# Kernel tuning notes

Hardware: AMD Instinct MI355X
Metric: run time of the kernel (lower is better)

## Reference

```python
import jax, jax.numpy as jnp
import numpy as np

B, H, W, D = 2, 64, 64, 512
D_HEAD = 64
N_HEADS = D // D_HEAD
KERNEL = 7


def make_neighbourhood_mask(kernel: int, canvas_h: int, canvas_w: int) -> jnp.ndarray:
    """Boolean [HW, HW] mask: query (i,j) attends to a clamped kernel x kernel window."""
    h_ramp = jnp.arange(canvas_h)
    w_ramp = jnp.arange(canvas_w)
    h_pos, w_pos = jnp.meshgrid(h_ramp, w_ramp, indexing='ij')
    start_h = jnp.clip(h_pos - kernel // 2, 0, canvas_h - kernel)[..., None, None]
    end_h = start_h + kernel
    start_w = jnp.clip(w_pos - kernel // 2, 0, canvas_w - kernel)[..., None, None]
    end_w = start_w + kernel
    h_range = h_ramp.reshape(1, 1, canvas_h, 1)
    w_range = w_ramp.reshape(1, 1, 1, canvas_w)
    mask = (h_range >= start_h) & (h_range < end_h) & (w_range >= start_w) & (w_range < end_w)
    return mask.reshape(canvas_h * canvas_w, canvas_h * canvas_w)


def setup_inputs() -> dict:
    key = jax.random.key(0)
    k1, k2, k3 = jax.random.split(key, 3)
    x = jax.random.normal(k1, (B, H, W, D), dtype=jnp.float32)
    w_qkv = jax.random.normal(k2, (3 * D, D), dtype=jnp.float32) * (D ** -0.5)
    w_out = jax.random.normal(k3, (D, D), dtype=jnp.float32) * (D ** -0.5)
    return {"x": x, "w_qkv": w_qkv, "w_out": w_out}


def reference(x, w_qkv, w_out):
    b, h, w, d = x.shape
    s = h * w
    # qkv projection (Linear, no bias): [b,h,w,3d]
    qkv = jnp.einsum('bhwd,ed->bhwe', x, w_qkv)
    # split per torch rearrange 'n h w (t nh e) -> t n nh (h w) e'
    qkv = qkv.reshape(b, s, 3, N_HEADS, D_HEAD).transpose(2, 0, 3, 1, 4)  # [3,b,nh,s,e]
    q, k, v = qkv[0], qkv[1], qkv[2]
    mask = make_neighbourhood_mask(KERNEL, h, w)  # [s, s] bool
    scale = D_HEAD ** -0.5
    scores = jnp.einsum('bnse,bnte->bnst', q, k) * scale  # [b,nh,s,s]
    neg_inf = jnp.finfo(scores.dtype).min
    scores = jnp.where(mask[None, None, :, :], scores, neg_inf)
    attn = jax.nn.softmax(scores, axis=-1)
    out = jnp.einsum('bnst,bnte->bnse', attn, v)  # [b,nh,s,e]
    out = out.transpose(0, 2, 1, 3).reshape(b, h, w, d)  # [b,h,w,d]
    return jnp.einsum('bhwd,ed->bhwe', out, w_out)
```

## Files before the change

kernel.cpp:

```cpp
#include <hip/hip_runtime.h>
#include <hip/hip_bf16.h>


typedef __bf16 bf16x8 __attribute__((ext_vector_type(8)));
typedef __bf16 bf16x4 __attribute__((ext_vector_type(4)));
typedef float  f32x4  __attribute__((ext_vector_type(4)));

__global__ __launch_bounds__(256) void cvt_w(
    const float* __restrict__ wq, const float* __restrict__ wo,
    __bf16* __restrict__ wqb, __bf16* __restrict__ wob) {
  int i = blockIdx.x * 256 + threadIdx.x;
  const float* src;
  __bf16* dst;
  int j = i;
  if (j < 196608) {
    src = wq; dst = wqb;
  } else {
    j -= 196608; src = wo; dst = wob;
  }
  f32x4 v = ((const f32x4*)src)[j];
  bf16x4 o;
  o[0] = (__bf16)v[0]; o[1] = (__bf16)v[1];
  o[2] = (__bf16)v[2]; o[3] = (__bf16)v[3];
  ((bf16x4*)dst)[j] = o;
}

__device__ __forceinline__ void gload_lds16(const __bf16* g, __bf16* l) {
  __builtin_amdgcn_global_load_lds(
      (const __attribute__((address_space(1))) void*)g,
      (__attribute__((address_space(3))) void*)l, 16, 0, 0);
}

__global__ __launch_bounds__(256, 3) void gemm_qkv(
    const float* __restrict__ A, const __bf16* __restrict__ W,
    __bf16* __restrict__ qo, __bf16* __restrict__ ko, __bf16* __restrict__ vo,
    int etiles) {
  constexpr int K = 512;
  __shared__ alignas(16) __bf16 Al[128][36];
  __shared__ alignas(16) __bf16 Wl[128 * 32];
  const int tid = threadIdx.x;
  const int wv = tid >> 6, lane = tid & 63;
  const int n16 = lane & 15, quad = lane >> 4;
  const int bi = blockIdx.x / etiles, be = blockIdx.x % etiles;
  const int i0 = bi << 7, e0 = be << 7;
  const int wm = (wv & 1) << 6, we = (wv >> 1) << 6;

  const int arow = tid >> 1, ahalf = tid & 1;
  const float* gA = A + (size_t)(i0 + arow) * K + ahalf * 16;
  const int srow = (wv << 4) + (lane >> 2);
  const int scol = (lane & 3) << 3;
  const __bf16* gW = W + (size_t)(e0 + srow) * K + scol;
  __bf16* lW = &Wl[(wv << 9) + (lane << 3)];

  f32x4 acc[4][4];
#pragma unroll
  for (int a = 0; a < 4; ++a)
#pragma unroll
    for (int b = 0; b < 4; ++b) acc[a][b] = (f32x4){0.f, 0.f, 0.f, 0.f};

  f32x4 a4[4];
#pragma unroll
  for (int j = 0; j < 4; ++j) a4[j] = *(const f32x4*)(gA + j * 4);

  for (int k0 = 0; k0 < K; k0 += 32) {
    bf16x8 ab0, ab1;
#pragma unroll
    for (int j = 0; j < 4; ++j) {
      ab0[j] = (__bf16)a4[0][j]; ab0[j + 4] = (__bf16)a4[1][j];
      ab1[j] = (__bf16)a4[2][j]; ab1[j + 4] = (__bf16)a4[3][j];
    }
    if (k0) __syncthreads();
    *(bf16x8*)&Al[arow][ahalf * 16] = ab0;
    *(bf16x8*)&Al[arow][ahalf * 16 + 8] = ab1;
    gload_lds16(gW + k0, lW);
    gload_lds16(gW + (size_t)64 * K + k0, lW + 64 * 32);
    if (k0 + 32 < K) {
#pragma unroll
      for (int j = 0; j < 4; ++j)
        a4[j] = *(const f32x4*)(gA + k0 + 32 + j * 4);
    }
    __syncthreads();

    bf16x8 af[4], wf[4];
#pragma unroll
    for (int t = 0; t < 4; ++t) {
      af[t] = *(const bf16x8*)&Al[wm + t * 16 + n16][quad * 8];
      wf[t] = *(const bf16x8*)&Wl[(we + t * 16 + n16) * 32 + quad * 8];
    }
#pragma unroll
    for (int mt = 0; mt < 4; ++mt)
#pragma unroll
      for (int nt = 0; nt < 4; ++nt)
        acc[mt][nt] = __builtin_amdgcn_mfma_f32_16x16x32_bf16(
            af[mt], wf[nt], acc[mt][nt], 0, 0, 0);
  }

#pragma unroll
  for (int mt = 0; mt < 4; ++mt)
#pragma unroll
    for (int nt = 0; nt < 4; ++nt) {
      f32x4 f = acc[mt][nt];
      int e = e0 + we + nt * 16 + n16;
      int t = e >> 9, head = (e >> 6) & 7, dh = e & 63;
      int ib = i0 + wm + mt * 16 + quad * 4;
      int b = ib >> 12, s = ib & 4095;
      int bh = b * 8 + head;
      if (t == 2) {
        __bf16* p = vo + ((size_t)bh * 64 + dh) * 4096 + s;
#pragma unroll
        for (int rg = 0; rg < 4; ++rg) p[rg] = (__bf16)f[rg];
      } else {
        __bf16* p = ((t == 0) ? qo : ko) + ((size_t)bh * 4096 + s) * 64 + dh;
#pragma unroll
        for (int rg = 0; rg < 4; ++rg) p[rg * 64] = (__bf16)f[rg];
      }
    }
}

__global__ __launch_bounds__(256, 3) void gemm_out(
    const __bf16* __restrict__ A, const __bf16* __restrict__ W,
    float* __restrict__ co, int etiles) {
  constexpr int K = 512;
  __shared__ alignas(16) __bf16 Al[128 * 32];
  __shared__ alignas(16) __bf16 Wl[64 * 32];
  const int tid = threadIdx.x;
  const int wv = tid >> 6, lane = tid & 63;
  const int n16 = lane & 15, quad = lane >> 4;
  const int bi = blockIdx.x / etiles, be = blockIdx.x % etiles;
  const int i0 = bi << 7, e0 = be << 6;
  const int wm = (wv & 1) << 6, we = (wv >> 1) << 5;

  const int srow = (wv << 4) + (lane >> 2);
  const int scol = (lane & 3) << 3;
  const __bf16* gA = A + (size_t)(i0 + srow) * K + scol;
  const __bf16* gW = W + (size_t)(e0 + srow) * K + scol;
  __bf16* lA = &Al[(wv << 9) + (lane << 3)];
  __bf16* lW = &Wl[(wv << 9) + (lane << 3)];

  f32x4 acc[4][2];
#pragma unroll
  for (int a = 0; a < 4; ++a)
#pragma unroll
    for (int b = 0; b < 2; ++b) acc[a][b] = (f32x4){0.f, 0.f, 0.f, 0.f};

  for (int k0 = 0; k0 < K; k0 += 32) {
    if (k0) __syncthreads();
    gload_lds16(gA + k0, lA);
    gload_lds16(gA + (size_t)64 * K + k0, lA + 64 * 32);
    gload_lds16(gW + k0, lW);
    __syncthreads();

    bf16x8 af[4], wf[2];
#pragma unroll
    for (int t = 0; t < 4; ++t)
      af[t] = *(const bf16x8*)&Al[(wm + t * 16 + n16) * 32 + quad * 8];
#pragma unroll
    for (int t = 0; t < 2; ++t)
      wf[t] = *(const bf16x8*)&Wl[(we + t * 16 + n16) * 32 + quad * 8];
#pragma unroll
    for (int mt = 0; mt < 4; ++mt)
#pragma unroll
      for (int nt = 0; nt < 2; ++nt)
        acc[mt][nt] = __builtin_amdgcn_mfma_f32_16x16x32_bf16(
            af[mt], wf[nt], acc[mt][nt], 0, 0, 0);
  }

#pragma unroll
  for (int mt = 0; mt < 4; ++mt)
#pragma unroll
    for (int nt = 0; nt < 2; ++nt) {
      f32x4 f = acc[mt][nt];
      int e = e0 + we + nt * 16 + n16;
      int ib = i0 + wm + mt * 16 + quad * 4;
      float* p = co + (size_t)ib * 512 + e;
#pragma unroll
      for (int rg = 0; rg < 4; ++rg) p[rg * 512] = f[rg];
    }
}

__global__ __launch_bounds__(256) void attn_mfma(
    const __bf16* __restrict__ q, const __bf16* __restrict__ k,
    const __bf16* __restrict__ vt, __bf16* __restrict__ out) {
  __shared__ alignas(16) __bf16 r1[14848];
  __shared__ alignas(16) __bf16 sbuf[4][16][232];
  const int tid = threadIdx.x;
  const int wv = tid >> 6;
  const int lane = tid & 63;
  const int n16 = lane & 15, quad = lane >> 4;
  const int bh = blockIdx.x >> 6;
  const int tile = blockIdx.x & 63;
  const int qh0 = (tile >> 3) << 3, qw0 = (tile & 7) << 3;
  int wh0 = qh0 - 3; wh0 = wh0 < 0 ? 0 : (wh0 > 50 ? 50 : wh0);
  int wc0 = qw0 - 3; wc0 = wc0 < 0 ? 0 : (wc0 > 48 ? 48 : wc0);
  wc0 &= ~1;
  const size_t base = (size_t)bh * 4096 * 64;

  const int qi_a = wv * 16 + n16;
  const int sqa = (qh0 + (qi_a >> 3)) * 64 + qw0 + (qi_a & 7);
  const __bf16* qp = q + base + (size_t)sqa * 64 + quad * 8;
  bf16x8 aq0 = *(const bf16x8*)qp;
  bf16x8 aq1 = *(const bf16x8*)(qp + 32);

  const __bf16* kbase = k + base;
#pragma unroll
  for (int i = 0; i < 7; ++i) {
    int ch = i * 256 + tid;
    int kr = ch >> 7, wi = ch & 127;
    int kc = wi >> 3, dh8 = wi & 7;
    bf16x8 d = *(const bf16x8*)(kbase +
        (size_t)((wh0 + kr) * 64 + wc0 + kc) * 64 + dh8 * 8);
    *(bf16x8*)&r1[(kr * 16 + kc) * 64 + ((dh8 ^ (kc & 7)) * 8)] = d;
  }
  __syncthreads();

  f32x4 S[14];
  const int skw = wc0 + n16;
  const int sw1 = ((quad ^ (n16 & 7)) * 8);
  const int sw2 = (((4 + quad) ^ (n16 & 7)) * 8);
#pragma unroll
  for (int nt = 0; nt < 14; ++nt) {
    int key = nt * 16 + n16;
    bf16x8 b0 = *(const bf16x8*)&r1[key * 64 + sw1];
    bf16x8 b1 = *(const bf16x8*)&r1[key * 64 + sw2];
    f32x4 s = {0.f, 0.f, 0.f, 0.f};
    s = __builtin_amdgcn_mfma_f32_16x16x32_bf16(aq0, b0, s, 0, 0, 0);
    s = __builtin_amdgcn_mfma_f32_16x16x32_bf16(aq1, b1, s, 0, 0, 0);
    S[nt] = s;
  }

  float mx[4] = {-1e30f, -1e30f, -1e30f, -1e30f};
#pragma unroll
  for (int reg = 0; reg < 4; ++reg) {
    int qi = wv * 16 + quad * 4 + reg;
    int qh = qh0 + (qi >> 3), qw = qw0 + (qi & 7);
    int sh = qh - 3; sh = sh < 0 ? 0 : (sh > 57 ? 57 : sh);
    int sw = qw - 3; sw = sw < 0 ? 0 : (sw > 57 ? 57 : sw);
    bool wok = (skw >= sw) && (skw < sw + 7);
#pragma unroll
    for (int nt = 0; nt < 14; ++nt) {
      int kh = wh0 + nt;
      bool ok = wok && (kh >= sh) && (kh < sh + 7);
      float val = ok ? S[nt][reg] * 0.125f : -1e30f;
      S[nt][reg] = val;
      mx[reg] = mx[reg] > val ? mx[reg] : val;
    }
  }
#pragma unroll
  for (int reg = 0; reg < 4; ++reg)
#pragma unroll
    for (int off = 8; off >= 1; off >>= 1) {
      float o = __shfl_xor(mx[reg], off);
      mx[reg] = mx[reg] > o ? mx[reg] : o;
    }

  float sm[4] = {0.f, 0.f, 0.f, 0.f};
#pragma unroll
  for (int nt = 0; nt < 14; ++nt)
#pragma unroll
    for (int reg = 0; reg < 4; ++reg) {
      float p = __expf(S[nt][reg] - mx[reg]);
      S[nt][reg] = p;
      sm[reg] += p;
    }
#pragma unroll
  for (int reg = 0; reg < 4; ++reg)
#pragma unroll
    for (int off = 8; off >= 1; off >>= 1) sm[reg] += __shfl_xor(sm[reg], off);

#pragma unroll
  for (int reg = 0; reg < 4; ++reg) {
    float inv = 1.f / sm[reg];
    int row = quad * 4 + reg;
#pragma unroll
    for (int nt = 0; nt < 14; ++nt)
      sbuf[wv][row][nt * 16 + n16] = (__bf16)(S[nt][reg] * inv);
  }

  __syncthreads();
  const __bf16* vtb = vt + base;
#pragma unroll
  for (int i = 0; i < 7; ++i) {
    int c = i * 256 + tid;
    int dh = c / 28, rem = c % 28;
    int kr = rem >> 1, half = rem & 1;
    bf16x8 d = *(const bf16x8*)(vtb + (size_t)dh * 4096 +
                                (wh0 + kr) * 64 + wc0 + half * 8);
    *(bf16x8*)&r1[dh * 232 + kr * 16 + half * 8] = d;
  }
  __syncthreads();

  f32x4 O[4] = {{0.f, 0.f, 0.f, 0.f},
                {0.f, 0.f, 0.f, 0.f},
                {0.f, 0.f, 0.f, 0.f},
                {0.f, 0.f, 0.f, 0.f}};
#pragma unroll
  for (int kt = 0; kt < 7; ++kt) {
    bf16x8 pa = *(const bf16x8*)&sbuf[wv][n16][kt * 32 + quad * 8];
    int key0 = kt * 32 + quad * 8;
#pragma unroll
    for (int ntv = 0; ntv < 4; ++ntv) {
      bf16x8 vb = *(const bf16x8*)&r1[(ntv * 16 + n16) * 232 + key0];
      O[ntv] = __builtin_amdgcn_mfma_f32_16x16x32_bf16(pa, vb, O[ntv], 0, 0, 0);
    }
  }

  const int b = bh >> 3, head = bh & 7;
#pragma unroll
  for (int ntv = 0; ntv < 4; ++ntv)
#pragma unroll
    for (int reg = 0; reg < 4; ++reg) {
      int qi = wv * 16 + quad * 4 + reg;
      int s_q = (qh0 + (qi >> 3)) * 64 + qw0 + (qi & 7);
      int dh = ntv * 16 + n16;
      out[((size_t)(b * 4096 + s_q)) * 512 + head * 64 + dh] =
          (__bf16)O[ntv][reg];
    }
}

extern "C" void kernel_launch(void* const* d_in, const int* in_sizes, int n_in,
                              void* d_out, int out_size, void* d_ws,
                              size_t ws_size, hipStream_t stream) {
  const float* x = (const float*)d_in[0];
  const float* w_qkv = (const float*)d_in[1];
  const float* w_out = (const float*)d_in[2];
  float* out = (float*)d_out;

  const size_t qelems = (size_t)2 * 8 * 4096 * 64;
  __bf16* q = (__bf16*)d_ws;
  __bf16* k = q + qelems;
  __bf16* vt = k + qelems;
  __bf16* ao = vt + qelems;
  __bf16* wqb = ao + qelems;
  __bf16* wob = wqb + 1536 * 512;

  cvt_w<<<dim3(1024), dim3(256), 0, stream>>>(w_qkv, w_out, wqb, wob);

  gemm_qkv<<<dim3(768), dim3(256), 0, stream>>>(x, wqb, q, k, vt, 12);
  attn_mfma<<<dim3(1024), dim3(256), 0, stream>>>(q, k, vt, ao);
  gemm_out<<<dim3(512), dim3(256), 0, stream>>>(ao, wob, out, 8);
}
```

Baseline: 141.2 us.

## Fuse all stages into one cooperative persistent kernel with grid syncs

Replaces the four launches (weight conversion, QKV GEMM, attention, output GEMM) with one cooperative persistent kernel that separates phases with grid.sync. It also converts x to bf16 up front so the QKV GEMM can load both operands straight to LDS, and it splits the K and V staging in the attention phase into smaller chunks so a shared LDS union fits 3 blocks per CU. This removes launch gaps and tail effects between kernels. In exchange it adds grid-wide barriers, an extra pass over x, and fewer resident blocks than the original grids, which can cost parallelism.

```diff
diff --git a/kernel.cpp b/kernel.cpp
--- a/kernel.cpp
+++ b/kernel.cpp
@@ -1,29 +1,13 @@
 #include <hip/hip_runtime.h>
 #include <hip/hip_bf16.h>
+#include <hip/hip_cooperative_groups.h>
+
+namespace cg = cooperative_groups;
 
 
 typedef __bf16 bf16x8 __attribute__((ext_vector_type(8)));
 typedef __bf16 bf16x4 __attribute__((ext_vector_type(4)));
 typedef float  f32x4  __attribute__((ext_vector_type(4)));
-
-__global__ __launch_bounds__(256) void cvt_w(
-    const float* __restrict__ wq, const float* __restrict__ wo,
-    __bf16* __restrict__ wqb, __bf16* __restrict__ wob) {
-  int i = blockIdx.x * 256 + threadIdx.x;
-  const float* src;
-  __bf16* dst;
-  int j = i;
-  if (j < 196608) {
-    src = wq; dst = wqb;
-  } else {
-    j -= 196608; src = wo; dst = wob;
-  }
-  f32x4 v = ((const f32x4*)src)[j];
-  bf16x4 o;
-  o[0] = (__bf16)v[0]; o[1] = (__bf16)v[1];
-  o[2] = (__bf16)v[2]; o[3] = (__bf16)v[3];
-  ((bf16x4*)dst)[j] = o;
-}
 
 __device__ __forceinline__ void gload_lds16(const __bf16* g, __bf16* l) {
   __builtin_amdgcn_global_load_lds(
@@ -31,290 +15,321 @@
       (__attribute__((address_space(3))) void*)l, 16, 0, 0);
 }
 
-__global__ __launch_bounds__(256, 3) void gemm_qkv(
-    const float* __restrict__ A, const __bf16* __restrict__ W,
-    __bf16* __restrict__ qo, __bf16* __restrict__ ko, __bf16* __restrict__ vo,
-    int etiles) {
-  constexpr int K = 512;
-  __shared__ alignas(16) __bf16 Al[128][36];
-  __shared__ alignas(16) __bf16 Wl[128 * 32];
+union SmemU {
+  struct { __bf16 Al[128 * 32]; __bf16 Wl[128 * 32]; } g;
+  struct { __bf16 r1[8192]; __bf16 P[4][16][232]; } a;
+};
+
+__global__ __launch_bounds__(256, 3) void mega(
+    const float* __restrict__ x, const float* __restrict__ wq,
+    const float* __restrict__ wo, float* __restrict__ out,
+    __bf16* __restrict__ qb, __bf16* __restrict__ kb,
+    __bf16* __restrict__ vtb, __bf16* __restrict__ xb,
+    __bf16* __restrict__ ao, __bf16* __restrict__ wqb,
+    __bf16* __restrict__ wob) {
+  __shared__ SmemU sm;
+  cg::grid_group grid = cg::this_grid();
   const int tid = threadIdx.x;
+  const int bid = blockIdx.x;
+  const int gsz = gridDim.x;
   const int wv = tid >> 6, lane = tid & 63;
   const int n16 = lane & 15, quad = lane >> 4;
-  const int bi = blockIdx.x / etiles, be = blockIdx.x % etiles;
-  const int i0 = bi << 7, e0 = be << 7;
-  const int wm = (wv & 1) << 6, we = (wv >> 1) << 6;
-
-  const int arow = tid >> 1, ahalf = tid & 1;
-  const float* gA = A + (size_t)(i0 + arow) * K + ahalf * 16;
-  const int srow = (wv << 4) + (lane >> 2);
-  const int scol = (lane & 3) << 3;
-  const __bf16* gW = W + (size_t)(e0 + srow) * K + scol;
-  __bf16* lW = &Wl[(wv << 9) + (lane << 3)];
-
-  f32x4 acc[4][4];
-#pragma unroll
-  for (int a = 0; a < 4; ++a)
-#pragma unroll
-    for (int b = 0; b < 4; ++b) acc[a][b] = (f32x4){0.f, 0.f, 0.f, 0.f};
-
-  f32x4 a4[4];
-#pragma unroll
-  for (int j = 0; j < 4; ++j) a4[j] = *(const f32x4*)(gA + j * 4);
-
-  for (int k0 = 0; k0 < K; k0 += 32) {
-    bf16x8 ab0, ab1;
-#pragma unroll
-    for (int j = 0; j < 4; ++j) {
-      ab0[j] = (__bf16)a4[0][j]; ab0[j + 4] = (__bf16)a4[1][j];
-      ab1[j] = (__bf16)a4[2][j]; ab1[j + 4] = (__bf16)a4[3][j];
-    }
-    if (k0) __syncthreads();
-    *(bf16x8*)&Al[arow][ahalf * 16] = ab0;
-    *(bf16x8*)&Al[arow][ahalf * 16 + 8] = ab1;
-    gload_lds16(gW + k0, lW);
-    gload_lds16(gW + (size_t)64 * K + k0, lW + 64 * 32);
-    if (k0 + 32 < K) {
-#pragma unroll
-      for (int j = 0; j < 4; ++j)
-        a4[j] = *(const f32x4*)(gA + k0 + 32 + j * 4);
-    }
+
+  {
+    const int gthreads = gsz << 8;
+    for (int c = (bid << 8) + tid; c < 1310720; c += gthreads) {
+      const float* src; __bf16* dst; int j = c;
+      if (j < 1048576) { src = x; dst = xb; }
+      else if (j < 1245184) { j -= 1048576; src = wq; dst = wqb; }
+      else { j -= 1245184; src = wo; dst = wob; }
+      f32x4 v = ((const f32x4*)src)[j];
+      bf16x4 o;
+      o[0] = (__bf16)v[0]; o[1] = (__bf16)v[1];
+      o[2] = (__bf16)v[2]; o[3] = (__bf16)v[3];
+      ((bf16x4*)dst)[j] = o;
+    }
+  }
+  __threadfence();
+  grid.sync();
+
+  {
+    constexpr int K = 512;
+    const int srow = (wv << 4) + (lane >> 2);
+    const int scol = (lane & 3) << 3;
+    __bf16* lA = &sm.g.Al[(wv << 9) + (lane << 3)];
+    __bf16* lW = &sm.g.Wl[(wv << 9) + (lane << 3)];
+    const int wm = (wv & 1) << 6, we = (wv >> 1) << 6;
+
+    for (int t = bid; t < 768; t += gsz) {
+      const int bi = t / 12, be = t % 12;
+      const int i0 = bi << 7, e0 = be << 7;
+      const __bf16* gA = xb + (size_t)(i0 + srow) * K + scol;
+      const __bf16* gW = wqb + (size_t)(e0 + srow) * K + scol;
+
+      f32x4 acc[4][4];
+#pragma unroll
+      for (int a = 0; a < 4; ++a)
+#pragma unroll
+        for (int b = 0; b < 4; ++b) acc[a][b] = (f32x4){0.f, 0.f, 0.f, 0.f};
+
+      for (int k0 = 0; k0 < K; k0 += 32) {
+        __syncthreads();
+        gload_lds16(gA + k0, lA);
+        gload_lds16(gA + (size_t)64 * K + k0, lA + 64 * 32);
+        gload_lds16(gW + k0, lW);
+        gload_lds16(gW + (size_t)64 * K + k0, lW + 64 * 32);
+        __syncthreads();
+
+        bf16x8 af[4], wf[4];
+#pragma unroll
+        for (int tt = 0; tt < 4; ++tt) {
+          af[tt] = *(const bf16x8*)&sm.g.Al[(wm + tt * 16 + n16) * 32 + quad * 8];
+          wf[tt] = *(const bf16x8*)&sm.g.Wl[(we + tt * 16 + n16) * 32 + quad * 8];
+        }
+#pragma unroll
+        for (int mt = 0; mt < 4; ++mt)
+#pragma unroll
+          for (int nt = 0; nt < 4; ++nt)
+            acc[mt][nt] = __builtin_amdgcn_mfma_f32_16x16x32_bf16(
+                af[mt], wf[nt], acc[mt][nt], 0, 0, 0);
+      }
+
+#pragma unroll
+      for (int mt = 0; mt < 4; ++mt)
+#pragma unroll
+        for (int nt = 0; nt < 4; ++nt) {
+          f32x4 f = acc[mt][nt];
+          int e = e0 + we + nt * 16 + n16;
+          int ty = e >> 9, head = (e >> 6) & 7, dh = e & 63;
+          int ib = i0 + wm + mt * 16 + quad * 4;
+          int b = ib >> 12, s = ib & 4095;
+          int bh = b * 8 + head;
+          if (ty == 2) {
+            __bf16* p = vtb + ((size_t)bh * 64 + dh) * 4096 + s;
+#pragma unroll
+            for (int rg = 0; rg < 4; ++rg) p[rg] = (__bf16)f[rg];
+          } else {
+            __bf16* p = ((ty == 0) ? qb : kb) + ((size_t)bh * 4096 + s) * 64 + dh;
+#pragma unroll
+            for (int rg = 0; rg < 4; ++rg) p[rg * 64] = (__bf16)f[rg];
+          }
+        }
+    }
+  }
+  __threadfence();
+  grid.sync();
+
+  for (int t = bid; t < 1024; t += gsz) {
+    const int bh = t >> 6;
+    const int tile = t & 63;
+    const int qh0 = (tile >> 3) << 3, qw0 = (tile & 7) << 3;
+    int wh0 = qh0 - 3; wh0 = wh0 < 0 ? 0 : (wh0 > 50 ? 50 : wh0);
+    int wc0 = qw0 - 3; wc0 = wc0 < 0 ? 0 : (wc0 > 48 ? 48 : wc0);
+    wc0 &= ~1;
+    const size_t base = (size_t)bh * 4096 * 64;
+
+    const int qi_a = wv * 16 + n16;
+    const int sqa = (qh0 + (qi_a >> 3)) * 64 + qw0 + (qi_a & 7);
+    const __bf16* qp = qb + base + (size_t)sqa * 64 + quad * 8;
+    bf16x8 aq0 = *(const bf16x8*)qp;
+    bf16x8 aq1 = *(const bf16x8*)(qp + 32);
+
+    const __bf16* kbase = kb + base;
+    const int skw = wc0 + n16;
+    const int sw1 = ((quad ^ (n16 & 7)) * 8);
+    const int sw2 = (((4 + quad) ^ (n16 & 7)) * 8);
+    f32x4 S[14];
+
     __syncthreads();
-
-    bf16x8 af[4], wf[4];
-#pragma unroll
-    for (int t = 0; t < 4; ++t) {
-      af[t] = *(const bf16x8*)&Al[wm + t * 16 + n16][quad * 8];
-      wf[t] = *(const bf16x8*)&Wl[(we + t * 16 + n16) * 32 + quad * 8];
-    }
-#pragma unroll
-    for (int mt = 0; mt < 4; ++mt)
-#pragma unroll
-      for (int nt = 0; nt < 4; ++nt)
-        acc[mt][nt] = __builtin_amdgcn_mfma_f32_16x16x32_bf16(
-            af[mt], wf[nt], acc[mt][nt], 0, 0, 0);
-  }
-
-#pragma unroll
-  for (int mt = 0; mt < 4; ++mt)
-#pragma unroll
-    for (int nt = 0; nt < 4; ++nt) {
-      f32x4 f = acc[mt][nt];
-      int e = e0 + we + nt * 16 + n16;
-      int t = e >> 9, head = (e >> 6) & 7, dh = e & 63;
-      int ib = i0 + wm + mt * 16 + quad * 4;
-      int b = ib >> 12, s = ib & 4095;
-      int bh = b * 8 + head;
-      if (t == 2) {
-        __bf16* p = vo + ((size_t)bh * 64 + dh) * 4096 + s;
-#pragma unroll
-        for (int rg = 0; rg < 4; ++rg) p[rg] = (__bf16)f[rg];
-      } else {
-        __bf16* p = ((t == 0) ? qo : ko) + ((size_t)bh * 4096 + s) * 64 + dh;
-#pragma unroll
-        for (int rg = 0; rg < 4; ++rg) p[rg * 64] = (__bf16)f[rg];
-      }
-    }
-}
-
-__global__ __launch_bounds__(256, 3) void gemm_out(
-    const __bf16* __restrict__ A, const __bf16* __restrict__ W,
-    float* __restrict__ co, int etiles) {
-  constexpr int K = 512;
-  __shared__ alignas(16) __bf16 Al[128 * 32];
-  __shared__ alignas(16) __bf16 Wl[64 * 32];
-  const int tid = threadIdx.x;
-  const int wv = tid >> 6, lane = tid & 63;
-  const int n16 = lane & 15, quad = lane >> 4;
-  const int bi = blockIdx.x / etiles, be = blockIdx.x % etiles;
-  const int i0 = bi << 7, e0 = be << 6;
-  const int wm = (wv & 1) << 6, we = (wv >> 1) << 5;
-
-  const int srow = (wv << 4) + (lane >> 2);
-  const int scol = (lane & 3) << 3;
-  const __bf16* gA = A + (size_t)(i0 + srow) * K + scol;
-  const __bf16* gW = W + (size_t)(e0 + srow) * K + scol;
-  __bf16* lA = &Al[(wv << 9) + (lane << 3)];
-  __bf16* lW = &Wl[(wv << 9) + (lane << 3)];
-
-  f32x4 acc[4][2];
-#pragma unroll
-  for (int a = 0; a < 4; ++a)
-#pragma unroll
-    for (int b = 0; b < 2; ++b) acc[a][b] = (f32x4){0.f, 0.f, 0.f, 0.f};
-
-  for (int k0 = 0; k0 < K; k0 += 32) {
-    if (k0) __syncthreads();
-    gload_lds16(gA + k0, lA);
-    gload_lds16(gA + (size_t)64 * K + k0, lA + 64 * 32);
-    gload_lds16(gW + k0, lW);
+#pragma unroll
+    for (int i = 0; i < 4; ++i) {
+      int ch = i * 256 + tid;
+      int kr = ch >> 7, wi = ch & 127;
+      int kc = wi >> 3, dh8 = wi & 7;
+      bf16x8 d = *(const bf16x8*)(kbase +
+          (size_t)((wh0 + kr) * 64 + wc0 + kc) * 64 + dh8 * 8);
+      *(bf16x8*)&sm.a.r1[(kr * 16 + kc) * 64 + ((dh8 ^ (kc & 7)) * 8)] = d;
+    }
     __syncthreads();
-
-    bf16x8 af[4], wf[2];
-#pragma unroll
-    for (int t = 0; t < 4; ++t)
-      af[t] = *(const bf16x8*)&Al[(wm + t * 16 + n16) * 32 + quad * 8];
-#pragma unroll
-    for (int t = 0; t < 2; ++t)
-      wf[t] = *(const bf16x8*)&Wl[(we + t * 16 + n16) * 32 + quad * 8];
-#pragma unroll
-    for (int mt = 0; mt < 4; ++mt)
-#pragma unroll
-      for (int nt = 0; nt < 2; ++nt)
-        acc[mt][nt] = __builtin_amdgcn_mfma_f32_16x16x32_bf16(
-            af[mt], wf[nt], acc[mt][nt], 0, 0, 0);
-  }
-
-#pragma unroll
-  for (int mt = 0; mt < 4; ++mt)
-#pragma unroll
-    for (int nt = 0; nt < 2; ++nt) {
-      f32x4 f = acc[mt][nt];
-      int e = e0 + we + nt * 16 + n16;
-      int ib = i0 + wm + mt * 16 + quad * 4;
-      float* p = co + (size_t)ib * 512 + e;
-#pragma unroll
-      for (int rg = 0; rg < 4; ++rg) p[rg * 512] = f[rg];
-    }
-}
-
-__global__ __launch_bounds__(256) void attn_mfma(
-    const __bf16* __restrict__ q, const __bf16* __restrict__ k,
-    const __bf16* __restrict__ vt, __bf16* __restrict__ out) {
-  __shared__ alignas(16) __bf16 r1[14848];
-  __shared__ alignas(16) __bf16 sbuf[4][16][232];
-  const int tid = threadIdx.x;
-  const int wv = tid >> 6;
-  const int lane = tid & 63;
-  const int n16 = lane & 15, quad = lane >> 4;
-  const int bh = blockIdx.x >> 6;
-  const int tile = blockIdx.x & 63;
-  const int qh0 = (tile >> 3) << 3, qw0 = (tile & 7) << 3;
-  int wh0 = qh0 - 3; wh0 = wh0 < 0 ? 0 : (wh0 > 50 ? 50 : wh0);
-  int wc0 = qw0 - 3; wc0 = wc0 < 0 ? 0 : (wc0 > 48 ? 48 : wc0);
-  wc0 &= ~1;
-  const size_t base = (size_t)bh * 4096 * 64;
-
-  const int qi_a = wv * 16 + n16;
-  const int sqa = (qh0 + (qi_a >> 3)) * 64 + qw0 + (qi_a & 7);
-  const __bf16* qp = q + base + (size_t)sqa * 64 + quad * 8;
-  bf16x8 aq0 = *(const bf16x8*)qp;
-  bf16x8 aq1 = *(const bf16x8*)(qp + 32);
-
-  const __bf16* kbase = k + base;
-#pragma unroll
-  for (int i = 0; i < 7; ++i) {
-    int ch = i * 256 + tid;
-    int kr = ch >> 7, wi = ch & 127;
-    int kc = wi >> 3, dh8 = wi & 7;
-    bf16x8 d = *(const bf16x8*)(kbase +
-        (size_t)((wh0 + kr) * 64 + wc0 + kc) * 64 + dh8 * 8);
-    *(bf16x8*)&r1[(kr * 16 + kc) * 64 + ((dh8 ^ (kc & 7)) * 8)] = d;
-  }
-  __syncthreads();
-
-  f32x4 S[14];
-  const int skw = wc0 + n16;
-  const int sw1 = ((quad ^ (n16 & 7)) * 8);
-  const int sw2 = (((4 + quad) ^ (n16 & 7)) * 8);
-#pragma unroll
-  for (int nt = 0; nt < 14; ++nt) {
-    int key = nt * 16 + n16;
-    bf16x8 b0 = *(const bf16x8*)&r1[key * 64 + sw1];
-    bf16x8 b1 = *(const bf16x8*)&r1[key * 64 + sw2];
-    f32x4 s = {0.f, 0.f, 0.f, 0.f};
-    s = __builtin_amdgcn_mfma_f32_16x16x32_bf16(aq0, b0, s, 0, 0, 0);
-    s = __builtin_amdgcn_mfma_f32_16x16x32_bf16(aq1, b1, s, 0, 0, 0);
-    S[nt] = s;
-  }
-
-  float mx[4] = {-1e30f, -1e30f, -1e30f, -1e30f};
-#pragma unroll
-  for (int reg = 0; reg < 4; ++reg) {
-    int qi = wv * 16 + quad * 4 + reg;
-    int qh = qh0 + (qi >> 3), qw = qw0 + (qi & 7);
-    int sh = qh - 3; sh = sh < 0 ? 0 : (sh > 57 ? 57 : sh);
-    int sw = qw - 3; sw = sw < 0 ? 0 : (sw > 57 ? 57 : sw);
-    bool wok = (skw >= sw) && (skw < sw + 7);
-#pragma unroll
-    for (int nt = 0; nt < 14; ++nt) {
-      int kh = wh0 + nt;
-      bool ok = wok && (kh >= sh) && (kh < sh + 7);
-      float val = ok ? S[nt][reg] * 0.125f : -1e30f;
-      S[nt][reg] = val;
-      mx[reg] = mx[reg] > val ? mx[reg] : val;
-    }
-  }
-#pragma unroll
-  for (int reg = 0; reg < 4; ++reg)
-#pragma unroll
-    for (int off = 8; off >= 1; off >>= 1) {
-      float o = __shfl_xor(mx[reg], off);
-      mx[reg] = mx[reg] > o ? mx[reg] : o;
-    }
-
-  float sm[4] = {0.f, 0.f, 0.f, 0.f};
-#pragma unroll
-  for (int nt = 0; nt < 14; ++nt)
-#pragma unroll
-    for (int reg = 0; reg < 4; ++reg) {
-      float p = __expf(S[nt][reg] - mx[reg]);
-      S[nt][reg] = p;
-      sm[reg] += p;
-    }
-#pragma unroll
-  for (int reg = 0; reg < 4; ++reg)
-#pragma unroll
-    for (int off = 8; off >= 1; off >>= 1) sm[reg] += __shfl_xor(sm[reg], off);
-
-#pragma unroll
-  for (int reg = 0; reg < 4; ++reg) {
-    float inv = 1.f / sm[reg];
-    int row = quad * 4 + reg;
-#pragma unroll
-    for (int nt = 0; nt < 14; ++nt)
-      sbuf[wv][row][nt * 16 + n16] = (__bf16)(S[nt][reg] * inv);
-  }
-
-  __syncthreads();
-  const __bf16* vtb = vt + base;
-#pragma unroll
-  for (int i = 0; i < 7; ++i) {
-    int c = i * 256 + tid;
-    int dh = c / 28, rem = c % 28;
-    int kr = rem >> 1, half = rem & 1;
-    bf16x8 d = *(const bf16x8*)(vtb + (size_t)dh * 4096 +
-                                (wh0 + kr) * 64 + wc0 + half * 8);
-    *(bf16x8*)&r1[dh * 232 + kr * 16 + half * 8] = d;
-  }
-  __syncthreads();
-
-  f32x4 O[4] = {{0.f, 0.f, 0.f, 0.f},
-                {0.f, 0.f, 0.f, 0.f},
-                {0.f, 0.f, 0.f, 0.f},
-                {0.f, 0.f, 0.f, 0.f}};
-#pragma unroll
-  for (int kt = 0; kt < 7; ++kt) {
-    bf16x8 pa = *(const bf16x8*)&sbuf[wv][n16][kt * 32 + quad * 8];
-    int key0 = kt * 32 + quad * 8;
-#pragma unroll
-    for (int ntv = 0; ntv < 4; ++ntv) {
-      bf16x8 vb = *(const bf16x8*)&r1[(ntv * 16 + n16) * 232 + key0];
-      O[ntv] = __builtin_amdgcn_mfma_f32_16x16x32_bf16(pa, vb, O[ntv], 0, 0, 0);
-    }
-  }
-
-  const int b = bh >> 3, head = bh & 7;
-#pragma unroll
-  for (int ntv = 0; ntv < 4; ++ntv)
+#pragma unroll
+    for (int nt = 0; nt < 8; ++nt) {
+      int key = nt * 16 + n16;
+      bf16x8 b0 = *(const bf16x8*)&sm.a.r1[key * 64 + sw1];
+      bf16x8 b1 = *(const bf16x8*)&sm.a.r1[key * 64 + sw2];
+      f32x4 s = {0.f, 0.f, 0.f, 0.f};
+      s = __builtin_amdgcn_mfma_f32_16x16x32_bf16(aq0, b0, s, 0, 0, 0);
+      s = __builtin_amdgcn_mfma_f32_16x16x32_bf16(aq1, b1, s, 0, 0, 0);
+      S[nt] = s;
+    }
+    __syncthreads();
+#pragma unroll
+    for (int i = 0; i < 3; ++i) {
+      int ch = i * 256 + tid;
+      int kr = ch >> 7, wi = ch & 127;
+      int kc = wi >> 3, dh8 = wi & 7;
+      bf16x8 d = *(const bf16x8*)(kbase +
+          (size_t)((wh0 + 8 + kr) * 64 + wc0 + kc) * 64 + dh8 * 8);
+      *(bf16x8*)&sm.a.r1[(kr * 16 + kc) * 64 + ((dh8 ^ (kc & 7)) * 8)] = d;
+    }
+    __syncthreads();
+#pragma unroll
+    for (int nt = 0; nt < 6; ++nt) {
+      int key = nt * 16 + n16;
+      bf16x8 b0 = *(const bf16x8*)&sm.a.r1[key * 64 + sw1];
+      bf16x8 b1 = *(const bf16x8*)&sm.a.r1[key * 64 + sw2];
+      f32x4 s = {0.f, 0.f, 0.f, 0.f};
+      s = __builtin_amdgcn_mfma_f32_16x16x32_bf16(aq0, b0, s, 0, 0, 0);
+      s = __builtin_amdgcn_mfma_f32_16x16x32_bf16(aq1, b1, s, 0, 0, 0);
+      S[8 + nt] = s;
+    }
+
+    float mx[4] = {-1e30f, -1e30f, -1e30f, -1e30f};
 #pragma unroll
     for (int reg = 0; reg < 4; ++reg) {
       int qi = wv * 16 + quad * 4 + reg;
-      int s_q = (qh0 + (qi >> 3)) * 64 + qw0 + (qi & 7);
-      int dh = ntv * 16 + n16;
-      out[((size_t)(b * 4096 + s_q)) * 512 + head * 64 + dh] =
-          (__bf16)O[ntv][reg];
-    }
+      int qh = qh0 + (qi >> 3), qw = qw0 + (qi & 7);
+      int sh = qh - 3; sh = sh < 0 ? 0 : (sh > 57 ? 57 : sh);
+      int sw = qw - 3; sw = sw < 0 ? 0 : (sw > 57 ? 57 : sw);
+      bool wok = (skw >= sw) && (skw < sw + 7);
+#pragma unroll
+      for (int nt = 0; nt < 14; ++nt) {
+        int kh = wh0 + nt;
+        bool ok = wok && (kh >= sh) && (kh < sh + 7);
+        float val = ok ? S[nt][reg] * 0.125f : -1e30f;
+        S[nt][reg] = val;
+        mx[reg] = mx[reg] > val ? mx[reg] : val;
+      }
+    }
+#pragma unroll
+    for (int reg = 0; reg < 4; ++reg)
+#pragma unroll
+      for (int off = 8; off >= 1; off >>= 1) {
+        float o = __shfl_xor(mx[reg], off);
+        mx[reg] = mx[reg] > o ? mx[reg] : o;
+      }
+
+    float smr[4] = {0.f, 0.f, 0.f, 0.f};
+#pragma unroll
+    for (int nt = 0; nt < 14; ++nt)
+#pragma unroll
+      for (int reg = 0; reg < 4; ++reg) {
+        float p = __expf(S[nt][reg] - mx[reg]);
+        S[nt][reg] = p;
+        smr[reg] += p;
+      }
+#pragma unroll
+    for (int reg = 0; reg < 4; ++reg)
+#pragma unroll
+      for (int off = 8; off >= 1; off >>= 1) smr[reg] += __shfl_xor(smr[reg], off);
+
+#pragma unroll
+    for (int reg = 0; reg < 4; ++reg) {
+      float inv = 1.f / smr[reg];
+      int row = quad * 4 + reg;
+#pragma unroll
+      for (int nt = 0; nt < 14; ++nt)
+        sm.a.P[wv][row][nt * 16 + n16] = (__bf16)(S[nt][reg] * inv);
+    }
+
+    const __bf16* vbase = vtb + base;
+    f32x4 O[4];
+#pragma unroll
+    for (int h = 0; h < 2; ++h) {
+      __syncthreads();
+#pragma unroll
+      for (int i = 0; i < 7; ++i) {
+        int c = i * 256 + tid;
+        int dh = c / 56, rem = c % 56;
+        int kr = rem >> 2, qtr = rem & 3;
+        bf16x4 d = *(const bf16x4*)(vbase + (size_t)(h * 32 + dh) * 4096 +
+                                    (wh0 + kr) * 64 + wc0 + qtr * 4);
+        *(bf16x4*)&sm.a.r1[dh * 232 + kr * 16 + qtr * 4] = d;
+      }
+      __syncthreads();
+#pragma unroll
+      for (int ntv = 0; ntv < 2; ++ntv) {
+        int oi = h * 2 + ntv;
+        O[oi] = (f32x4){0.f, 0.f, 0.f, 0.f};
+#pragma unroll
+        for (int kt = 0; kt < 7; ++kt) {
+          bf16x8 pa = *(const bf16x8*)&sm.a.P[wv][n16][kt * 32 + quad * 8];
+          bf16x8 vb = *(const bf16x8*)&sm.a.r1[(ntv * 16 + n16) * 232 +
+                                               kt * 32 + quad * 8];
+          O[oi] = __builtin_amdgcn_mfma_f32_16x16x32_bf16(pa, vb, O[oi], 0, 0, 0);
+        }
+      }
+    }
+
+    const int b = bh >> 3, head = bh & 7;
+#pragma unroll
+    for (int oi = 0; oi < 4; ++oi)
+#pragma unroll
+      for (int reg = 0; reg < 4; ++reg) {
+        int qi = wv * 16 + quad * 4 + reg;
+        int s_q = (qh0 + (qi >> 3)) * 64 + qw0 + (qi & 7);
+        int dh = oi * 16 + n16;
+        ao[((size_t)(b * 4096 + s_q)) * 512 + head * 64 + dh] =
+            (__bf16)O[oi][reg];
+      }
+  }
+  __threadfence();
+  grid.sync();
+
+  {
+    constexpr int K = 512;
+    const int srow = (wv << 4) + (lane >> 2);
+    const int scol = (lane & 3) << 3;
+    __bf16* lA = &sm.g.Al[(wv << 9) + (lane << 3)];
+    __bf16* lW = &sm.g.Wl[(wv << 9) + (lane << 3)];
+    const int wm = (wv & 1) << 6, we = (wv >> 1) << 5;
+
+    for (int t = bid; t < 512; t += gsz) {
+      const int bi = t >> 3, be = t & 7;
+      const int i0 = bi << 7, e0 = be << 6;
+      const __bf16* gA = ao + (size_t)(i0 + srow) * K + scol;
+      const __bf16* gW = wob + (size_t)(e0 + srow) * K + scol;
+
+      f32x4 acc[4][2];
+#pragma unroll
+      for (int a = 0; a < 4; ++a)
+#pragma unroll
+        for (int b = 0; b < 2; ++b) acc[a][b] = (f32x4){0.f, 0.f, 0.f, 0.f};
+
+      for (int k0 = 0; k0 < K; k0 += 32) {
+        __syncthreads();
+        gload_lds16(gA + k0, lA);
+        gload_lds16(gA + (size_t)64 * K + k0, lA + 64 * 32);
+        gload_lds16(gW + k0, lW);
+        __syncthreads();
+
+        bf16x8 af[4], wf[2];
+#pragma unroll
+        for (int tt = 0; tt < 4; ++tt)
+          af[tt] = *(const bf16x8*)&sm.g.Al[(wm + tt * 16 + n16) * 32 + quad * 8];
+#pragma unroll
+        for (int tt = 0; tt < 2; ++tt)
+          wf[tt] = *(const bf16x8*)&sm.g.Wl[(we + tt * 16 + n16) * 32 + quad * 8];
+#pragma unroll
+        for (int mt = 0; mt < 4; ++mt)
+#pragma unroll
+          for (int nt = 0; nt < 2; ++nt)
+            acc[mt][nt] = __builtin_amdgcn_mfma_f32_16x16x32_bf16(
+                af[mt], wf[nt], acc[mt][nt], 0, 0, 0);
+      }
+
+#pragma unroll
+      for (int mt = 0; mt < 4; ++mt)
+#pragma unroll
+        for (int nt = 0; nt < 2; ++nt) {
+          f32x4 f = acc[mt][nt];
+          int e = e0 + we + nt * 16 + n16;
+          int ib = i0 + wm + mt * 16 + quad * 4;
+          float* p = out + (size_t)ib * 512 + e;
+#pragma unroll
+          for (int rg = 0; rg < 4; ++rg) p[rg * 512] = f[rg];
+        }
+    }
+  }
 }
 
 extern "C" void kernel_launch(void* const* d_in, const int* in_sizes, int n_in,
@@ -329,13 +344,22 @@
   __bf16* q = (__bf16*)d_ws;
   __bf16* k = q + qelems;
   __bf16* vt = k + qelems;
-  __bf16* ao = vt + qelems;
-  __bf16* wqb = ao + qelems;
+  __bf16* xb = vt + qelems;
+  __bf16* ao = xb;
+  __bf16* wqb = xb + qelems;
   __bf16* wob = wqb + 1536 * 512;
 
-  cvt_w<<<dim3(1024), dim3(256), 0, stream>>>(w_qkv, w_out, wqb, wob);
-
-  gemm_qkv<<<dim3(768), dim3(256), 0, stream>>>(x, wqb, q, k, vt, 12);
-  attn_mfma<<<dim3(1024), dim3(256), 0, stream>>>(q, k, vt, ao);
-  gemm_out<<<dim3(512), dim3(256), 0, stream>>>(ao, wob, out, 8);
+  int nb = 0;
+  if (hipOccupancyMaxActiveBlocksPerMultiprocessor(&nb, (const void*)mega,
+                                                   256, 0) != hipSuccess ||
+      nb < 1)
+    nb = 2;
+  int gridn = nb * 256;
+  if (gridn > 768) gridn = 768;
+
+  void* args[] = {(void*)&x,  (void*)&w_qkv, (void*)&w_out, (void*)&out,
+                  (void*)&q,  (void*)&k,     (void*)&vt,    (void*)&xb,
+                  (void*)&ao, (void*)&wqb,   (void*)&wob};
+  hipLaunchCooperativeKernel((const void*)mega, dim3(gridn), dim3(256), args,
+                             0, stream);
 }
```

Result: slower. 362.5 us (+156.7%).
